# Performance work log

Measured on AMD Instinct MI355X. Metric: run time of the kernel, lower is better.

## Reference

```python
import jax, jax.numpy as jnp
import numpy as np

B, S, LQ = 32, 1024, 128
EMB = 256; H = 256; NH = 8; DH = H // NH
NCATE, NCONT, NNODE = 4, 8, 4
VOCAB = 50000
EPS = 1e-5
LK = S - LQ


def _ln(x, g, b):
    mu = jnp.mean(x, -1, keepdims=True)
    xc = x - mu
    var = jnp.mean(xc * xc, -1, keepdims=True)
    return xc * jax.lax.rsqrt(var + EPS) * g + b


def _leaky(x):
    return jnp.where(x >= 0, x, 0.01 * x)  # LeakyReLU slope 0.01 (torch default)


def setup_inputs() -> dict:
    key = jax.random.key(0)
    ks = jax.random.split(key, 48)
    rnd = lambda i, shape, scale=0.02: jax.random.normal(ks[i], shape, dtype=jnp.float32) * scale
    rng = np.random.default_rng(0)
    qidx = jnp.asarray(np.sort(rng.choice(S, LQ, replace=False)).astype(np.int64))
    cate_table = rnd(6, (VOCAB, EMB)).at[0].set(0.0)  # padding_idx=0
    inp = {
        "node": jax.random.normal(ks[0], (B, S, EMB * NNODE), dtype=jnp.float32),
        "cate": jax.random.randint(ks[1], (B, S, NCATE), 0, VOCAB),
        "cont": jax.random.normal(ks[2], (B, S, NCONT), dtype=jnp.float32),
        "query_index": qidx,
        "mask": jax.random.bernoulli(ks[3], 0.1, (B, LK)),
        "cate_table": cate_table,
        "pos_emb": rnd(4, (1, S, H)),
        "node_W": rnd(5, (EMB * NNODE, H)), "node_b": jnp.zeros((H,), jnp.float32),
        "node_ln_g": jnp.ones((H,), jnp.float32), "node_ln_b": jnp.zeros((H,), jnp.float32),
        "cate_W": rnd(7, (EMB * NCATE, H)), "cate_b": jnp.zeros((H,), jnp.float32),
        "cate_ln_g": jnp.ones((H,), jnp.float32), "cate_ln_b": jnp.zeros((H,), jnp.float32),
        "bn_g": jnp.ones((NCONT,), jnp.float32), "bn_b": jnp.zeros((NCONT,), jnp.float32),
        "cont_W": rnd(8, (NCONT, H)), "cont_b": jnp.zeros((H,), jnp.float32),
        "cont_ln_g": jnp.ones((H,), jnp.float32), "cont_ln_b": jnp.zeros((H,), jnp.float32),
        "comb_W": rnd(9, (3 * H, H)), "comb_b": jnp.zeros((H,), jnp.float32),
        "comb_ln_g": jnp.ones((H,), jnp.float32), "comb_ln_b": jnp.zeros((H,), jnp.float32),
        "q_W": rnd(10, (H, H)), "q_b": jnp.zeros((H,), jnp.float32),
        "k_W": rnd(11, (H, H)), "k_b": jnp.zeros((H,), jnp.float32),
        "v_W": rnd(12, (H, H)), "v_b": jnp.zeros((H,), jnp.float32),
        "reg_W1": rnd(13, (H, H)), "reg_b1": jnp.zeros((H,), jnp.float32),
        "reg_ln_g": jnp.ones((H,), jnp.float32), "reg_ln_b": jnp.zeros((H,), jnp.float32),
        "reg_W2": rnd(14, (H, H)), "reg_b2": jnp.zeros((H,), jnp.float32),
    }
    return inp


def reference(node, cate, cont, query_index, mask, cate_table, pos_emb,
              node_W, node_b, node_ln_g, node_ln_b,
              cate_W, cate_b, cate_ln_g, cate_ln_b,
              bn_g, bn_b, cont_W, cont_b, cont_ln_g, cont_ln_b,
              comb_W, comb_b, comb_ln_g, comb_ln_b,
              q_W, q_b, k_W, k_b, v_W, v_b,
              reg_W1, reg_b1, reg_ln_g, reg_ln_b, reg_W2, reg_b2):
    # --- three embedding branches: Linear -> LayerNorm ---
    node_e = _ln(node @ node_W + node_b, node_ln_g, node_ln_b)
    ce = cate_table[cate].reshape(B, S, NCATE * EMB)  # embedding gather
    cate_e = _ln(ce @ cate_W + cate_b, cate_ln_g, cate_ln_b)
    # BatchNorm1d (training-mode batch stats, biased var) over flattened [B*S, C]
    cf = cont.reshape(-1, NCONT)
    mu = jnp.mean(cf, 0)
    var = jnp.mean((cf - mu) ** 2, 0)
    cn = ((cf - mu) * jax.lax.rsqrt(var + EPS) * bn_g + bn_b).reshape(B, S, NCONT)
    cont_e = _ln(cn @ cont_W + cont_b, cont_ln_g, cont_ln_b)
    # --- combine + positions ---
    seq = jnp.concatenate([node_e, cate_e, cont_e], -1)       # [B,S,3H]
    seq = _ln(_leaky(seq) @ comb_W + comb_b, comb_ln_g, comb_ln_b) + pos_emb  # [B,S,H]
    # --- gather-split cross attention: queries vs complement keys ---
    is_q = jnp.zeros((S,), bool).at[query_index].set(True)
    key_index = jnp.nonzero(~is_q, size=LK)[0]                # setdiff1d, static size
    q = seq[:, query_index]                                   # [B,LQ,H]
    kv = seq[:, key_index]                                    # [B,LK,H]
    Q = (q @ q_W + q_b).reshape(B, LQ, NH, DH).transpose(0, 2, 1, 3)
    K = (kv @ k_W + k_b).reshape(B, LK, NH, DH).transpose(0, 2, 1, 3)
    V = (kv @ v_W + v_b).reshape(B, LK, NH, DH).transpose(0, 2, 1, 3)
    scale = jnp.float32(1.0 / np.sqrt(DH))
    scores = jnp.einsum('bhqd,bhkd->bhqk', Q, K) * scale      # [B,NH,LQ,LK]
    scores = jnp.where(mask[:, None, None, :], jnp.float32(-1e9), scores)
    attn = jax.nn.softmax(scores, -1)                         # dropout = identity (eval)
    out = jnp.einsum('bhqk,bhkd->bhqd', attn, V).transpose(0, 2, 1, 3).reshape(B, LQ, H)
    h = _leaky(_ln(out @ reg_W1 + reg_b1, reg_ln_g, reg_ln_b))
    return h @ reg_W2 + reg_b2                                # [B,LQ,H]
```

## Files before the change

kernel.cpp:

```cpp
#include <hip/hip_runtime.h>
#include <cstdint>

#define EPSV 1e-5f
#define AS1 __attribute__((address_space(1)))
#define AS3 __attribute__((address_space(3)))

#define VMCNT_BAR(N) do { \
    asm volatile("s_waitcnt vmcnt(" #N ") lgkmcnt(0)" ::: "memory"); \
    __builtin_amdgcn_sched_barrier(0); \
    __builtin_amdgcn_s_barrier(); } while (0)

typedef __attribute__((ext_vector_type(8))) short short8v;
typedef __attribute__((ext_vector_type(4))) float float4v;

__device__ inline unsigned short f2bf(float f) {
    union { float f; unsigned int u; } v; v.f = f;
    unsigned int r = v.u + 0x7FFF + ((v.u >> 16) & 1);
    return (unsigned short)(r >> 16);
}

__device__ inline size_t bidx(int n, int k) {
    return ((size_t)(k >> 5) << 13) + ((size_t)(n >> 4) << 9)
         + (((k >> 3) & 3) << 7) + ((n & 15) << 3) + (k & 7);
}

__device__ inline void gld16(const unsigned short* g, unsigned short* d) {
    __builtin_amdgcn_global_load_lds((const AS1 void*)g, (AS3 void*)d, 16, 0, 0);
}

__device__ inline void issue_b(const unsigned short* Bc, int s, unsigned short* bsb,
                               int w, int l) {
    const unsigned short* g = Bc + ((size_t)s << 13) + (w << 9) + (l << 3);
    unsigned short* d = bsb + (w << 9) + (l << 3);
    #pragma unroll
    for (int i = 0; i < 4; ++i)
        gld16(g + (i << 11), d + (i << 11));
}

__device__ inline void issue_b8(const unsigned short* Bc, int s, unsigned short* bsb,
                                int w, int l) {
    const unsigned short* g = Bc + ((size_t)(2 * s) << 13);
    #pragma unroll
    for (int i = 0; i < 4; ++i) {
        int blk = (w + i * 8) << 9;
        gld16(g + blk + (l << 3), bsb + blk + (l << 3));
    }
}

__global__ __launch_bounds__(256) void wt_all_k(
    const float* __restrict__ nW, const float* __restrict__ cW, const float* __restrict__ mW,
    const float* __restrict__ qW, const float* __restrict__ kW, const float* __restrict__ vW,
    const float* __restrict__ r1W, const float* __restrict__ r2W,
    unsigned short* __restrict__ nO, unsigned short* __restrict__ cO, unsigned short* __restrict__ mO,
    unsigned short* __restrict__ qO, unsigned short* __restrict__ kO, unsigned short* __restrict__ vO,
    unsigned short* __restrict__ r1O, unsigned short* __restrict__ r2O)
{
    __shared__ float T[64][65];
    int bid = blockIdx.x;
    const float* W; unsigned short* O; int K, tile;
    if (bid < 64)       { W = nW; O = nO; K = 1024; tile = bid; }
    else if (bid < 128) { W = cW; O = cO; K = 1024; tile = bid - 64; }
    else if (bid < 176) { W = mW; O = mO; K = 768;  tile = bid - 128; }
    else {
        int s = (bid - 176) >> 4; tile = (bid - 176) & 15; K = 256;
        switch (s) {
            case 0: W = qW;  O = qO;  break;
            case 1: W = kW;  O = kO;  break;
            case 2: W = vW;  O = vO;  break;
            case 3: W = r1W; O = r1O; break;
            default: W = r2W; O = r2O; break;
        }
    }
    int kTiles = K >> 6;
    int k0 = (tile % kTiles) * 64, n0 = (tile / kTiles) * 64;
    int c = threadIdx.x & 63, r4 = threadIdx.x >> 6;
    #pragma unroll
    for (int rr = 0; rr < 64; rr += 4) {
        int r = rr + r4;
        T[r][c] = W[(size_t)(k0 + r) * 256 + n0 + c];
    }
    __syncthreads();
    #pragma unroll
    for (int rr = 0; rr < 64; rr += 4) {
        int n = rr + r4;
        O[bidx(n0 + n, k0 + c)] = f2bf(T[c][n]);
    }
}

__global__ __launch_bounds__(512, 4) void gemm_nc_k(
    const float* __restrict__ node, const int* __restrict__ cate,
    const float* __restrict__ table,
    const unsigned short* __restrict__ nWt, const unsigned short* __restrict__ cWt,
    const float* __restrict__ nb, const float* __restrict__ cb,
    const float* __restrict__ nlg, const float* __restrict__ nlb,
    const float* __restrict__ clg, const float* __restrict__ clb,
    unsigned short* __restrict__ Y)
{
    __shared__ union UN {
        unsigned short A[2][4096];
        struct { float S[64][4]; float Q[64][4]; } red;
    } U;
    __shared__ unsigned short Bs[2][16384];
    const int t = threadIdx.x;
    const bool isC = blockIdx.x >= 512;
    const int bm = (isC ? (int)blockIdx.x - 512 : (int)blockIdx.x) * 64;
    const int w = t >> 6, l = t & 63, lr = l & 15, lg = l >> 4;
    const int wm = w >> 2, wn = w & 3;
    const int ar = t >> 3;
    const int ac = (t & 7) * 8;
    const int aw = ((ac >> 5) << 11) + ((ar >> 4) << 9)
                 + (((ac >> 3) & 3) << 7) + ((ar & 15) << 3);

    const unsigned short* Bc = isC ? cWt : nWt;
    const float* bias = isC ? cb : nb;
    const float* lng  = isC ? clg : nlg;
    const float* lnbp = isC ? clb : nlb;
    const int colOff = isC ? 256 : 0;

    const float* apf = node + (size_t)(bm + ar) * 1024 + ac;
    int4 idx4 = {0,0,0,0};
    if (isC) idx4 = *(const int4*)&cate[(bm + ar) * 4];

    float4v acc[2][4];
    #pragma unroll
    for (int i = 0; i < 2; ++i)
        #pragma unroll
        for (int j = 0; j < 4; ++j) acc[i][j] = (float4v)0.f;

    float4 rA0, rA1;

    auto loadA = [&](int s) {
        const float* p;
        if (isC) {
            int kt = s * 64 + ac;
            int g = kt >> 8;
            int idx = (g == 0) ? idx4.x : (g == 1) ? idx4.y : (g == 2) ? idx4.z : idx4.w;
            p = table + (size_t)idx * 256 + (kt & 255);
        } else {
            p = apf + s * 64;
        }
        rA0 = *(const float4*)p;
        rA1 = *(const float4*)(p + 4);
    };
    auto writeA = [&](unsigned short* Ab) {
        short8v v;
        v[0] = (short)f2bf(rA0.x); v[1] = (short)f2bf(rA0.y);
        v[2] = (short)f2bf(rA0.z); v[3] = (short)f2bf(rA0.w);
        v[4] = (short)f2bf(rA1.x); v[5] = (short)f2bf(rA1.y);
        v[6] = (short)f2bf(rA1.z); v[7] = (short)f2bf(rA1.w);
        *(short8v*)&Ab[aw] = v;
    };
    auto comp = [&](const unsigned short* Ab, const unsigned short* bsb) {
        #pragma unroll
        for (int kk = 0; kk < 2; ++kk) {
            short8v af[2], bf[4];
            #pragma unroll
            for (int i = 0; i < 2; ++i)
                af[i] = *(const short8v*)&Ab[kk*2048 + ((wm*2 + i) << 9) + (lg << 7) + (lr << 3)];
            #pragma unroll
            for (int j = 0; j < 4; ++j)
                bf[j] = *(const short8v*)&bsb[kk*8192 + ((wn*4 + j) << 9) + (lg << 7) + (lr << 3)];
            #pragma unroll
            for (int i = 0; i < 2; ++i)
                #pragma unroll
                for (int j = 0; j < 4; ++j)
                    acc[i][j] = __builtin_amdgcn_mfma_f32_16x16x32_bf16(af[i], bf[j], acc[i][j], 0, 0, 0);
        }
    };

    issue_b8(Bc, 0, &Bs[0][0], w, l);
    loadA(0);
    writeA(U.A[0]);
    VMCNT_BAR(0);

    for (int s = 0; s < 16; ++s) {
        const int cur = s & 1;
        if (s + 1 < 16) {
            issue_b8(Bc, s + 1, &Bs[1 - cur][0], w, l);
            loadA(s + 1);
        }
        __builtin_amdgcn_sched_barrier(0);
        comp(U.A[cur], &Bs[cur][0]);
        if (s + 1 < 16) {
            writeA(U.A[1 - cur]);
            VMCNT_BAR(0);
        }
    }

    #pragma unroll
    for (int j = 0; j < 4; ++j) {
        float bvj = bias[wn*64 + j*16 + lr];
        #pragma unroll
        for (int i = 0; i < 2; ++i)
            #pragma unroll
            for (int r4 = 0; r4 < 4; ++r4) acc[i][j][r4] += bvj;
    }
    __syncthreads();
    #pragma unroll
    for (int i = 0; i < 2; ++i) {
        float ps[4], qs[4];
        #pragma unroll
        for (int r4 = 0; r4 < 4; ++r4) {
            float a0 = acc[i][0][r4], a1 = acc[i][1][r4],
                  a2 = acc[i][2][r4], a3 = acc[i][3][r4];
            ps[r4] = (a0 + a1) + (a2 + a3);
            qs[r4] = (a0*a0 + a1*a1) + (a2*a2 + a3*a3);
        }
        #pragma unroll
        for (int o = 1; o < 16; o <<= 1)
            #pragma unroll
            for (int r4 = 0; r4 < 4; ++r4) {
                ps[r4] += __shfl_xor(ps[r4], o);
                qs[r4] += __shfl_xor(qs[r4], o);
            }
        if (lr == 0) {
            #pragma unroll
            for (int r4 = 0; r4 < 4; ++r4) {
                int rlc = wm*32 + i*16 + lg*4 + r4;
                U.red.S[rlc][wn] = ps[r4];
                U.red.Q[rlc][wn] = qs[r4];
            }
        }
    }
    __syncthreads();
    #pragma unroll
    for (int i = 0; i < 2; ++i) {
        float mu[4], rstd[4];
        #pragma unroll
        for (int r4 = 0; r4 < 4; ++r4) {
            int rlc = wm*32 + i*16 + lg*4 + r4;
            float s  = (U.red.S[rlc][0] + U.red.S[rlc][1]) + (U.red.S[rlc][2] + U.red.S[rlc][3]);
            float qq = (U.red.Q[rlc][0] + U.red.Q[rlc][1]) + (U.red.Q[rlc][2] + U.red.Q[rlc][3]);
            float m_ = s * (1.0f/256.0f);
            mu[r4] = m_;
            rstd[r4] = rsqrtf(qq * (1.0f/256.0f) - m_*m_ + EPSV);
        }
        #pragma unroll
        for (int j = 0; j < 4; ++j) {
            int c = wn*64 + j*16 + lr;
            float gv = lng[c], b2 = lnbp[c];
            #pragma unroll
            for (int r4 = 0; r4 < 4; ++r4) {
                int row = bm + wm*32 + i*16 + lg*4 + r4;
                float y = (acc[i][j][r4] - mu[r4]) * rstd[r4] * gv + b2;
                y = (y >= 0.f) ? y : 0.01f*y;
                Y[(size_t)row * 768 + colOff + c] = f2bf(y);
            }
        }
    }
}

__global__ __launch_bounds__(512, 4) void gemm_comb_k(
    const unsigned short* __restrict__ A,
    const unsigned short* __restrict__ Bc,
    const float* __restrict__ bias,
    const float* __restrict__ lng, const float* __restrict__ lnbp,
    const float* __restrict__ pos,
    unsigned short* __restrict__ Y)
{
    __shared__ union UC {
        unsigned short A[2][4096];
        struct { float S[64][4]; float Q[64][4]; } red;
    } U;
    __shared__ unsigned short Bs[2][16384];
    const int t = threadIdx.x;
    const int bm = blockIdx.x * 64;
    const int w = t >> 6, l = t & 63, lr = l & 15, lg = l >> 4;
    const int wm = w >> 2, wn = w & 3;
    const int ar = t >> 3;
    const int ak = (t & 7) * 8;
    const int aw = ((ak >> 5) << 11) + ((ar >> 4) << 9)
                 + (((ak >> 3) & 3) << 7) + ((ar & 15) << 3);

    const unsigned short* ap = A + (size_t)(bm + ar) * 768 + ak;

    float4v acc[2][4];
    #pragma unroll
    for (int i = 0; i < 2; ++i)
        #pragma unroll
        for (int j = 0; j < 4; ++j) acc[i][j] = (float4v)0.f;

    short8v aA;

    auto comp = [&](const unsigned short* Ab, const unsigned short* bsb) {
        #pragma unroll
        for (int kk = 0; kk < 2; ++kk) {
            short8v af[2], bf[4];
            #pragma unroll
            for (int i = 0; i < 2; ++i)
                af[i] = *(const short8v*)&Ab[kk*2048 + ((wm*2 + i) << 9) + (lg << 7) + (lr << 3)];
            #pragma unroll
            for (int j = 0; j < 4; ++j)
                bf[j] = *(const short8v*)&bsb[kk*8192 + ((wn*4 + j) << 9) + (lg << 7) + (lr << 3)];
            #pragma unroll
            for (int i = 0; i < 2; ++i)
                #pragma unroll
                for (int j = 0; j < 4; ++j)
                    acc[i][j] = __builtin_amdgcn_mfma_f32_16x16x32_bf16(af[i], bf[j], acc[i][j], 0, 0, 0);
        }
    };

    issue_b8(Bc, 0, &Bs[0][0], w, l);
    aA = *(const short8v*)(ap);
    *(short8v*)&U.A[0][aw] = aA;
    VMCNT_BAR(0);

    for (int s = 0; s < 12; ++s) {
        const int cur = s & 1;
        if (s + 1 < 12) {
            issue_b8(Bc, s + 1, &Bs[1 - cur][0], w, l);
            aA = *(const short8v*)(ap + (s + 1) * 64);
        }
        __builtin_amdgcn_sched_barrier(0);
        comp(U.A[cur], &Bs[cur][0]);
        if (s + 1 < 12) {
            *(short8v*)&U.A[1 - cur][aw] = aA;
            VMCNT_BAR(0);
        }
    }

    #pragma unroll
    for (int j = 0; j < 4; ++j) {
        float bvj = bias[wn*64 + j*16 + lr];
        #pragma unroll
        for (int i = 0; i < 2; ++i)
            #pragma unroll
            for (int r4 = 0; r4 < 4; ++r4) acc[i][j][r4] += bvj;
    }
    __syncthreads();
    #pragma unroll
    for (int i = 0; i < 2; ++i) {
        float ps[4], qs[4];
        #pragma unroll
        for (int r4 = 0; r4 < 4; ++r4) {
            float a0 = acc[i][0][r4], a1 = acc[i][1][r4],
                  a2 = acc[i][2][r4], a3 = acc[i][3][r4];
            ps[r4] = (a0 + a1) + (a2 + a3);
            qs[r4] = (a0*a0 + a1*a1) + (a2*a2 + a3*a3);
        }
        #pragma unroll
        for (int o = 1; o < 16; o <<= 1)
            #pragma unroll
            for (int r4 = 0; r4 < 4; ++r4) {
                ps[r4] += __shfl_xor(ps[r4], o);
                qs[r4] += __shfl_xor(qs[r4], o);
            }
        if (lr == 0) {
            #pragma unroll
            for (int r4 = 0; r4 < 4; ++r4) {
                int rlc = wm*32 + i*16 + lg*4 + r4;
                U.red.S[rlc][wn] = ps[r4];
                U.red.Q[rlc][wn] = qs[r4];
            }
        }
    }
    __syncthreads();
    #pragma unroll
    for (int i = 0; i < 2; ++i) {
        float mu[4], rstd[4];
        #pragma unroll
        for (int r4 = 0; r4 < 4; ++r4) {
            int rlc = wm*32 + i*16 + lg*4 + r4;
            float s  = (U.red.S[rlc][0] + U.red.S[rlc][1]) + (U.red.S[rlc][2] + U.red.S[rlc][3]);
            float qq = (U.red.Q[rlc][0] + U.red.Q[rlc][1]) + (U.red.Q[rlc][2] + U.red.Q[rlc][3]);
            float m_ = s * (1.0f/256.0f);
            mu[r4] = m_;
            rstd[r4] = rsqrtf(qq * (1.0f/256.0f) - m_*m_ + EPSV);
        }
        #pragma unroll
        for (int j = 0; j < 4; ++j) {
            int c = wn*64 + j*16 + lr;
            float gv = lng[c], b2 = lnbp[c];
            #pragma unroll
            for (int r4 = 0; r4 < 4; ++r4) {
                int row = bm + wm*32 + i*16 + lg*4 + r4;
                float y = (acc[i][j][r4] - mu[r4]) * rstd[r4] * gv + b2
                        + pos[(size_t)(row & 1023) * 256 + c];
                Y[(size_t)row * 256 + c] = f2bf(y);
            }
        }
    }
}

__global__ __launch_bounds__(512, 4) void gemm_qkv_k(
    const unsigned short* __restrict__ seq,
    const int* __restrict__ qmap, const int* __restrict__ krmap,
    const unsigned short* __restrict__ qWt, const unsigned short* __restrict__ kWt,
    const unsigned short* __restrict__ vWt,
    const float* __restrict__ qb, const float* __restrict__ kb, const float* __restrict__ vb,
    unsigned short* __restrict__ Qo, unsigned short* __restrict__ Ko,
    unsigned short* __restrict__ Vt)
{
    __shared__ unsigned short Asl[2][4096];
    __shared__ unsigned short Bs[2][16384];
    const int t = threadIdx.x;
    const int bid = blockIdx.x;
    int seg, bm;
    const int* gmap; const unsigned short* Bc; const float* bias;
    if (bid < 64)       { seg = 0; bm = bid * 64;         gmap = qmap;  Bc = qWt; bias = qb; }
    else if (bid < 512) { seg = 1; bm = (bid - 64) * 64;  gmap = krmap; Bc = kWt; bias = kb; }
    else                { seg = 2; bm = (bid - 512) * 64; gmap = krmap; Bc = vWt; bias = vb; }
    const int w = t >> 6, l = t & 63, lr = l & 15, lg = l >> 4;
    const int wm = w >> 2, wn = w & 3;
    const int ar = t >> 3;
    const int ak = (t & 7) * 8;
    const int aw = ((ak >> 5) << 11) + ((ar >> 4) << 9)
                 + (((ak >> 3) & 3) << 7) + ((ar & 15) << 3);

    const unsigned short* ap = seq + (size_t)gmap[bm + ar] * 256 + ak;

    float4v acc[2][4];
    #pragma unroll
    for (int i = 0; i < 2; ++i)
        #pragma unroll
        for (int j = 0; j < 4; ++j) acc[i][j] = (float4v)0.f;

    short8v aA;

    auto comp = [&](const unsigned short* Ab, const unsigned short* bsb) {
        #pragma unroll
        for (int kk = 0; kk < 2; ++kk) {
            short8v af[2], bf[4];
            #pragma unroll
            for (int i = 0; i < 2; ++i)
                af[i] = *(const short8v*)&Ab[kk*2048 + ((wm*2 + i) << 9) + (lg << 7) + (lr << 3)];
            #pragma unroll
            for (int j = 0; j < 4; ++j)
                bf[j] = *(const short8v*)&bsb[kk*8192 + ((wn*4 + j) << 9) + (lg << 7) + (lr << 3)];
            #pragma unroll
            for (int i = 0; i < 2; ++i)
                #pragma unroll
                for (int j = 0; j < 4; ++j)
                    acc[i][j] = __builtin_amdgcn_mfma_f32_16x16x32_bf16(af[i], bf[j], acc[i][j], 0, 0, 0);
        }
    };

    issue_b8(Bc, 0, &Bs[0][0], w, l);
    aA = *(const short8v*)(ap);
    *(short8v*)&Asl[0][aw] = aA;
    VMCNT_BAR(0);

    for (int s = 0; s < 4; ++s) {
        const int cur = s & 1;
        if (s + 1 < 4) {
            issue_b8(Bc, s + 1, &Bs[1 - cur][0], w, l);
            aA = *(const short8v*)(ap + (s + 1) * 64);
        }
        __builtin_amdgcn_sched_barrier(0);
        comp(Asl[cur], &Bs[cur][0]);
        if (s + 1 < 4) {
            *(short8v*)&Asl[1 - cur][aw] = aA;
            VMCNT_BAR(0);
        }
    }

    unsigned short* outp = (seg == 0) ? Qo : (seg == 1) ? Ko : Vt;
    #pragma unroll
    for (int j = 0; j < 4; ++j) {
        int c = wn*64 + j*16 + lr;
        float bvj = bias[c];
        #pragma unroll
        for (int i = 0; i < 2; ++i) {
            #pragma unroll
            for (int r4 = 0; r4 < 4; ++r4) {
                int rl = wm*32 + i*16 + lg*4 + r4;
                float val = acc[i][j][r4] + bvj;
                if (seg < 2) {
                    outp[(size_t)(bm + rl) * 256 + c] = f2bf(val);
                } else {
                    int vbk = bm / 896;
                    int kl = bm - vbk * 896 + rl;
                    outp[((size_t)vbk * 256 + c) * 896 + kl] = f2bf(val);
                }
            }
        }
    }
}

template<int EPI>
__global__ __launch_bounds__(256) void gemm_reg_k(
    const unsigned short* __restrict__ Asrc,
    const unsigned short* __restrict__ Bc,
    const float* __restrict__ bias,
    const float* __restrict__ ln_g,
    const float* __restrict__ ln_b,
    void* __restrict__ Cout)
{
    __shared__ union UR {
        unsigned short A[2][4096];
        struct { float S[64][4]; float Q[64][4]; } red;
    } U;
    __shared__ unsigned short Bs[2][16384];
    const int t = threadIdx.x;
    const int bm = blockIdx.x * 64;
    const int w = t >> 6, l = t & 63, lr = l & 15, lg = l >> 4;
    const int ar = t >> 2;
    const int ac = (t & 3) * 16;
    const int aw0 = (((t & 3) >> 1) << 11) + ((ar >> 4) << 9)
                  + ((((t & 3) * 2) & 3) << 7) + ((ar & 15) << 3);
    const int aw1 = aw0 + 128;

    const unsigned short* ap = Asrc + (size_t)(bm + ar) * 256 + ac;

    float4v acc[4][4];
    #pragma unroll
    for (int i = 0; i < 4; ++i)
        #pragma unroll
        for (int j = 0; j < 4; ++j) acc[i][j] = (float4v)0.f;

    short8v a0A, a1A, a0B, a1B;

    auto comp = [&](const unsigned short* Ab, const unsigned short* bsb) {
        #pragma unroll
        for (int kk = 0; kk < 2; ++kk) {
            short8v af[4], bf[4];
            #pragma unroll
            for (int i = 0; i < 4; ++i)
                af[i] = *(const short8v*)&Ab[kk*2048 + i*512 + lg*128 + lr*8];
            #pragma unroll
            for (int j = 0; j < 4; ++j)
                bf[j] = *(const short8v*)&bsb[kk*8192 + ((w*4 + j) << 9) + (lg << 7) + (lr << 3)];
            #pragma unroll
            for (int i = 0; i < 4; ++i)
                #pragma unroll
                for (int j = 0; j < 4; ++j)
                    acc[i][j] = __builtin_amdgcn_mfma_f32_16x16x32_bf16(af[i], bf[j], acc[i][j], 0, 0, 0);
        }
    };

    issue_b(Bc, 0, &Bs[0][0], w, l);
    issue_b(Bc, 1, &Bs[0][8192], w, l);
    a0A = *(const short8v*)(ap);
    a1A = *(const short8v*)(ap + 8);
    for (int s = 0; s < 4; ++s) {
        int cur = s & 1;
        __syncthreads();
        *(short8v*)&U.A[cur][aw0] = a0A;
        *(short8v*)&U.A[cur][aw1] = a1A;
        __syncthreads();
        if (s + 1 < 4) {
            issue_b(Bc, 2*(s+1),     &Bs[1 - cur][0],    w, l);
            issue_b(Bc, 2*(s+1) + 1, &Bs[1 - cur][8192], w, l);
            a0B = *(const short8v*)(ap + (s + 1) * 64);
            a1B = *(const short8v*)(ap + (s + 1) * 64 + 8);
        }
        comp(U.A[cur], &Bs[cur][0]);
        a0A = a0B; a1A = a1B;
    }

    #pragma unroll
    for (int j = 0; j < 4; ++j) {
        float bvj = bias[w*64 + j*16 + lr];
        #pragma unroll
        for (int i = 0; i < 4; ++i)
            #pragma unroll
            for (int r4 = 0; r4 < 4; ++r4) acc[i][j][r4] += bvj;
    }

    if (EPI == 0) {
        #pragma unroll
        for (int i = 0; i < 4; ++i)
            #pragma unroll
            for (int j = 0; j < 4; ++j) {
                int c = w*64 + j*16 + lr;
                #pragma unroll
                for (int r4 = 0; r4 < 4; ++r4) {
                    int rl = i*16 + lg*4 + r4;
                    ((float*)Cout)[(size_t)(bm + rl) * 256 + c] = acc[i][j][r4];
                }
            }
    } else {
        __syncthreads();
        #pragma unroll
        for (int i = 0; i < 4; ++i) {
            float ps[4], qs[4];
            #pragma unroll
            for (int r4 = 0; r4 < 4; ++r4) {
                float a0 = acc[i][0][r4], a1 = acc[i][1][r4],
                      a2 = acc[i][2][r4], a3 = acc[i][3][r4];
                ps[r4] = (a0 + a1) + (a2 + a3);
                qs[r4] = (a0*a0 + a1*a1) + (a2*a2 + a3*a3);
            }
            #pragma unroll
            for (int o = 1; o < 16; o <<= 1)
                #pragma unroll
                for (int r4 = 0; r4 < 4; ++r4) {
                    ps[r4] += __shfl_xor(ps[r4], o);
                    qs[r4] += __shfl_xor(qs[r4], o);
                }
            if (lr == 0) {
                #pragma unroll
                for (int r4 = 0; r4 < 4; ++r4) {
                    U.red.S[i*16 + lg*4 + r4][w] = ps[r4];
                    U.red.Q[i*16 + lg*4 + r4][w] = qs[r4];
                }
            }
        }
        __syncthreads();
        #pragma unroll
        for (int i = 0; i < 4; ++i) {
            float mu[4], rstd[4];
            #pragma unroll
            for (int r4 = 0; r4 < 4; ++r4) {
                int rl = i*16 + lg*4 + r4;
                float s  = (U.red.S[rl][0] + U.red.S[rl][1]) + (U.red.S[rl][2] + U.red.S[rl][3]);
                float qq = (U.red.Q[rl][0] + U.red.Q[rl][1]) + (U.red.Q[rl][2] + U.red.Q[rl][3]);
                float m_ = s * (1.0f/256.0f);
                mu[r4] = m_;
                rstd[r4] = rsqrtf(qq * (1.0f/256.0f) - m_*m_ + EPSV);
            }
            #pragma unroll
            for (int j = 0; j < 4; ++j) {
                int c = w*64 + j*16 + lr;
                float gv = ln_g[c], b2 = ln_b[c];
                #pragma unroll
                for (int r4 = 0; r4 < 4; ++r4) {
                    int row = bm + i*16 + lg*4 + r4;
                    float y = (acc[i][j][r4] - mu[r4]) * rstd[r4] * gv + b2;
                    y = (y >= 0.f) ? y : 0.01f*y;
                    ((unsigned short*)Cout)[(size_t)row * 256 + c] = f2bf(y);
                }
            }
        }
    }
}

__global__ __launch_bounds__(256) void bn_stats_k(const float* __restrict__ cont,
                                                  float* __restrict__ stats)
{
    __shared__ float ss[8], sq[8];
    int tid = threadIdx.x;
    if (tid < 8) { ss[tid] = 0.f; sq[tid] = 0.f; }
    __syncthreads();
    int gt = blockIdx.x * 256 + tid;
    float s = 0.f, q = 0.f;
    for (int e = gt; e < 32768*8; e += 256*256) { float v = cont[e]; s += v; q += v*v; }
    int f = gt & 7;
    atomicAdd(&ss[f], s);
    atomicAdd(&sq[f], q);
    __syncthreads();
    if (tid < 8) { atomicAdd(&stats[tid], ss[tid]); atomicAdd(&stats[8+tid], sq[tid]); }
}

__global__ __launch_bounds__(256) void cont_k(
    const float* __restrict__ cont, const float* __restrict__ stats,
    const float* __restrict__ bn_g, const float* __restrict__ bn_b,
    const float* __restrict__ W, const float* __restrict__ bias,
    const float* __restrict__ g, const float* __restrict__ bL,
    unsigned short* __restrict__ seq3)
{
    __shared__ float Ws[8][256];
    __shared__ float sscale[8], sshift[8];
    __shared__ float cr[8];
    __shared__ float red[8];
    int tid = threadIdx.x;
    #pragma unroll
    for (int d = 0; d < 8; ++d) Ws[d][tid] = W[d*256 + tid];
    if (tid < 8) {
        float mean = stats[tid] * (1.0f/32768.0f);
        float var  = stats[8+tid] * (1.0f/32768.0f) - mean*mean;
        float r = rsqrtf(var + EPSV);
        float sc = r * bn_g[tid];
        sscale[tid] = sc;
        sshift[tid] = bn_b[tid] - mean*sc;
    }
    __syncthreads();
    int lane = tid & 63, wv = tid >> 6;
    float gv = g[tid], bv = bL[tid], biasv = bias[tid];
    for (int row = blockIdx.x; row < 32768; row += gridDim.x) {
        if (tid < 8) cr[tid] = cont[(size_t)row*8 + tid]*sscale[tid] + sshift[tid];
        __syncthreads();
        float acc = biasv;
        #pragma unroll
        for (int d = 0; d < 8; ++d) acc += cr[d]*Ws[d][tid];
        float s = acc;
        #pragma unroll
        for (int o = 32; o; o >>= 1) s += __shfl_xor(s, o);
        if (lane == 0) red[wv] = s;
        __syncthreads();
        float mu = (red[0]+red[1]+red[2]+red[3]) * (1.0f/256.0f);
        float dc = acc - mu;
        float qv = dc*dc;
        #pragma unroll
        for (int o = 32; o; o >>= 1) qv += __shfl_xor(qv, o);
        if (lane == 0) red[4+wv] = qv;
        __syncthreads();
        float var = (red[4]+red[5]+red[6]+red[7]) * (1.0f/256.0f);
        float y = dc * rsqrtf(var + EPSV) * gv + bv;
        y = (y >= 0.f) ? y : 0.01f*y;
        seq3[(size_t)row*768 + 512 + tid] = f2bf(y);
        __syncthreads();
    }
}

__global__ void build_maps_k(const int* __restrict__ qidx, int* __restrict__ kmap)
{
    __shared__ int flag[1024];
    __shared__ int scan[1024];
    int t = threadIdx.x;
    flag[t] = 0;
    __syncthreads();
    if (t < 128) flag[qidx[t]] = 1;
    __syncthreads();
    int nq = 1 - flag[t];
    scan[t] = nq;
    __syncthreads();
    for (int off = 1; off < 1024; off <<= 1) {
        int v = (t >= off) ? scan[t - off] : 0;
        __syncthreads();
        scan[t] += v;
        __syncthreads();
    }
    if (nq) kmap[scan[t] - 1] = t;
}

__global__ void expand_maps_k(const int* __restrict__ qidx, const int* __restrict__ kmap,
                              int* __restrict__ qmap, int* __restrict__ krmap)
{
    int i = blockIdx.x * 256 + threadIdx.x;
    if (i < 32*128) { int b = i >> 7; int t = i & 127; qmap[i] = b*1024 + qidx[t]; }
    if (i < 32*896) { int b = i / 896; int t = i - b*896; krmap[i] = b*1024 + kmap[t]; }
}

__global__ __launch_bounds__(256) void mask_sniff_k(const unsigned char* __restrict__ msrc,
                                                    int* __restrict__ flags)
{
    int i = blockIdx.x * 256 + threadIdx.x;
    unsigned char v = msrc[i];
    bool u8  = v && (i & 3);
    bool i32 = v && !(i & 3) && ((i & 7) == 4);
    unsigned long long bu = __ballot(u8);
    unsigned long long bi = __ballot(i32);
    if ((threadIdx.x & 63) == 0) {
        if (bu) atomicOr(&flags[0], 1);
        if (bi) atomicOr(&flags[1], 1);
    }
}

__global__ __launch_bounds__(256) void mask_conv_k(const unsigned char* __restrict__ msrc,
                                                   const int* __restrict__ flags,
                                                   unsigned char* __restrict__ mu8)
{
    int i = blockIdx.x * 256 + threadIdx.x;
    int mode = flags[0] ? 0 : (flags[1] ? 1 : 2);
    unsigned char v;
    if (mode == 0)      v = msrc[i] ? 1 : 0;
    else if (mode == 1) v = ((const int*)msrc)[i] ? 1 : 0;
    else                v = ((const long long*)msrc)[i] ? 1 : 0;
    mu8[i] = v;
}

__global__ __launch_bounds__(256) void attn_mfma_k(
    const unsigned short* __restrict__ Qb,
    const unsigned short* __restrict__ Kb,
    const unsigned short* __restrict__ Vtb,
    const unsigned char* __restrict__ mask,
    unsigned short* __restrict__ out)
{
    __shared__ unsigned short Pw[4][16][72];
    const int t = threadIdx.x;
    const int w = t >> 6, l = t & 63;
    const int lr = l & 15, lg = l >> 4;
    const int bx = blockIdx.x;
    const int qh = bx & 1, h = (bx >> 1) & 7, b = bx >> 4;
    const int qrow0 = b*128 + qh*64 + w*16;

    short8v qf = *(const short8v*)&Qb[(size_t)(qrow0 + lr)*256 + h*32 + lg*8];

    const unsigned short* Kbase = Kb + (size_t)b*896*256 + h*32;
    const unsigned short* Vbase = Vtb + ((size_t)b*256 + h*32)*896;
    const unsigned char* mrow = mask + b*896;

    float4v O0 = (float4v)0.f, O1 = (float4v)0.f;
    float m[4], lsum[4];
    #pragma unroll
    for (int r = 0; r < 4; ++r) { m[r] = -3.0e38f; lsum[r] = 0.f; }

    short8v kf[4], vf[4];
    int mk[4];
    #pragma unroll
    for (int i = 0; i < 4; ++i) {
        kf[i] = *(const short8v*)&Kbase[(size_t)(i*16 + lr)*256 + lg*8];
        mk[i] = mrow[i*16 + lr];
    }
    #pragma unroll
    for (int kc = 0; kc < 2; ++kc)
        #pragma unroll
        for (int nt = 0; nt < 2; ++nt)
            vf[kc*2+nt] = *(const short8v*)&Vbase[(size_t)(nt*16 + lr)*896 + kc*32 + lg*8];

    for (int kt3 = 0; kt3 < 14; ++kt3) {
        const int kb2 = kt3*64 + 64;
        short8v kf2[4], vf2[4];
        int mk2[4];
        if (kt3 < 13) {
            #pragma unroll
            for (int i = 0; i < 4; ++i) {
                kf2[i] = *(const short8v*)&Kbase[(size_t)(kb2 + i*16 + lr)*256 + lg*8];
                mk2[i] = mrow[kb2 + i*16 + lr];
            }
            #pragma unroll
            for (int kc = 0; kc < 2; ++kc)
                #pragma unroll
                for (int nt = 0; nt < 2; ++nt)
                    vf2[kc*2+nt] = *(const short8v*)&Vbase[(size_t)(nt*16 + lr)*896 + kb2 + kc*32 + lg*8];
        }
        float4v s4[4];
        #pragma unroll
        for (int i = 0; i < 4; ++i)
            s4[i] = __builtin_amdgcn_mfma_f32_16x16x32_bf16(qf, kf[i], (float4v)0.f, 0, 0, 0);
        #pragma unroll
        for (int i = 0; i < 4; ++i)
            #pragma unroll
            for (int r = 0; r < 4; ++r)
                s4[i][r] = mk[i] ? -1e9f : s4[i][r] * 0.17677669529663687f;
        float tm[4];
        #pragma unroll
        for (int r = 0; r < 4; ++r)
            tm[r] = fmaxf(fmaxf(s4[0][r], s4[1][r]), fmaxf(s4[2][r], s4[3][r]));
        #pragma unroll
        for (int o = 1; o < 16; o <<= 1)
            #pragma unroll
            for (int r = 0; r < 4; ++r) tm[r] = fmaxf(tm[r], __shfl_xor(tm[r], o));
        float resc[4];
        #pragma unroll
        for (int r = 0; r < 4; ++r) {
            float mn = fmaxf(m[r], tm[r]);
            resc[r] = __expf(m[r] - mn);
            m[r] = mn;
        }
        float rs[4] = {0.f, 0.f, 0.f, 0.f};
        #pragma unroll
        for (int i = 0; i < 4; ++i)
            #pragma unroll
            for (int r = 0; r < 4; ++r) {
                float p = __expf(s4[i][r] - m[r]);
                s4[i][r] = p;
                rs[r] += p;
            }
        #pragma unroll
        for (int o = 1; o < 16; o <<= 1)
            #pragma unroll
            for (int r = 0; r < 4; ++r) rs[r] += __shfl_xor(rs[r], o);
        #pragma unroll
        for (int r = 0; r < 4; ++r) lsum[r] = lsum[r]*resc[r] + rs[r];
        #pragma unroll
        for (int r = 0; r < 4; ++r) { O0[r] *= resc[r]; O1[r] *= resc[r]; }
        #pragma unroll
        for (int i = 0; i < 4; ++i)
            #pragma unroll
            for (int r = 0; r < 4; ++r)
                Pw[w][lg*4 + r][i*16 + lr] = f2bf(s4[i][r]);
        #pragma unroll
        for (int kc = 0; kc < 2; ++kc) {
            short8v pf = *(const short8v*)&Pw[w][lr][kc*32 + lg*8];
            O0 = __builtin_amdgcn_mfma_f32_16x16x32_bf16(pf, vf[kc*2+0], O0, 0, 0, 0);
            O1 = __builtin_amdgcn_mfma_f32_16x16x32_bf16(pf, vf[kc*2+1], O1, 0, 0, 0);
        }
        if (kt3 < 13) {
            #pragma unroll
            for (int i = 0; i < 4; ++i) { kf[i] = kf2[i]; mk[i] = mk2[i]; vf[i] = vf2[i]; }
        }
    }
    #pragma unroll
    for (int r = 0; r < 4; ++r) {
        float inv = 1.0f / lsum[r];
        size_t row = (size_t)(qrow0 + lg*4 + r);
        out[row*256 + h*32 + lr]      = f2bf(O0[r] * inv);
        out[row*256 + h*32 + 16 + lr] = f2bf(O1[r] * inv);
    }
}

extern "C" void kernel_launch(void* const* d_in, const int* in_sizes, int n_in,
                              void* d_out, int out_size, void* d_ws, size_t ws_size,
                              hipStream_t stream)
{
    const float* node       = (const float*)d_in[0];
    const int*   cate       = (const int*)d_in[1];
    const float* cont       = (const float*)d_in[2];
    const int*   qidx       = (const int*)d_in[3];
    const unsigned char* mask = (const unsigned char*)d_in[4];
    const float* cate_table = (const float*)d_in[5];
    const float* pos_emb    = (const float*)d_in[6];
    const float* node_W     = (const float*)d_in[7];
    const float* node_b     = (const float*)d_in[8];
    const float* node_ln_g  = (const float*)d_in[9];
    const float* node_ln_b  = (const float*)d_in[10];
    const float* cate_W     = (const float*)d_in[11];
    const float* cate_b     = (const float*)d_in[12];
    const float* cate_ln_g  = (const float*)d_in[13];
    const float* cate_ln_b  = (const float*)d_in[14];
    const float* bn_g       = (const float*)d_in[15];
    const float* bn_b       = (const float*)d_in[16];
    const float* cont_W     = (const float*)d_in[17];
    const float* cont_b     = (const float*)d_in[18];
    const float* cont_ln_g  = (const float*)d_in[19];
    const float* cont_ln_b  = (const float*)d_in[20];
    const float* comb_W     = (const float*)d_in[21];
    const float* comb_b     = (const float*)d_in[22];
    const float* comb_ln_g  = (const float*)d_in[23];
    const float* comb_ln_b  = (const float*)d_in[24];
    const float* q_W        = (const float*)d_in[25];
    const float* q_b        = (const float*)d_in[26];
    const float* k_W        = (const float*)d_in[27];
    const float* k_b        = (const float*)d_in[28];
    const float* v_W        = (const float*)d_in[29];
    const float* v_b        = (const float*)d_in[30];
    const float* reg_W1     = (const float*)d_in[31];
    const float* reg_b1     = (const float*)d_in[32];
    const float* reg_ln_g   = (const float*)d_in[33];
    const float* reg_ln_b   = (const float*)d_in[34];
    const float* reg_W2     = (const float*)d_in[35];
    const float* reg_b2     = (const float*)d_in[36];

    char* ws = (char*)d_ws;
    unsigned short* seq3bf = (unsigned short*)(ws + 0);
    unsigned short* seqbf  = (unsigned short*)(ws + 83886080);
    unsigned short* Qbf    = (unsigned short*)(ws + 100663296);
    unsigned short* Kbf    = (unsigned short*)(ws + 102760448);
    unsigned short* Vtbf   = (unsigned short*)(ws + 117440512);
    unsigned short* AObf   = (unsigned short*)(ws + 132120576);
    unsigned short* Hbf    = (unsigned short*)(ws + 0);
    float* stats = (float*)(ws + 165675008);
    int*   flags = (int*)  (ws + 165675072);
    int*   kmap  = (int*)  (ws + 165675136);
    int*   qmap  = (int*)  (ws + 165678720);
    int*   krmap = (int*)  (ws + 165695104);
    unsigned char* mu8 = (unsigned char*)(ws + 165809792);
    unsigned short* node_Wt = (unsigned short*)(ws + 165838464);
    unsigned short* cate_Wt = (unsigned short*)(ws + 166362752);
    unsigned short* comb_Wt = (unsigned short*)(ws + 166887040);
    unsigned short* q_Wt    = (unsigned short*)(ws + 167280256);
    unsigned short* k_Wt    = (unsigned short*)(ws + 167411328);
    unsigned short* v_Wt    = (unsigned short*)(ws + 167542400);
    unsigned short* r1_Wt   = (unsigned short*)(ws + 167673472);
    unsigned short* r2_Wt   = (unsigned short*)(ws + 167804544);
    float* outp = (float*)d_out;

    hipMemsetAsync(stats, 0, 128, stream);
    bn_stats_k<<<256, 256, 0, stream>>>(cont, stats);
    mask_sniff_k<<<112, 256, 0, stream>>>(mask, flags);
    mask_conv_k<<<112, 256, 0, stream>>>(mask, flags, mu8);
    wt_all_k<<<256, 256, 0, stream>>>(node_W, cate_W, comb_W, q_W, k_W, v_W, reg_W1, reg_W2,
                                      node_Wt, cate_Wt, comb_Wt, q_Wt, k_Wt, v_Wt, r1_Wt, r2_Wt);

    gemm_nc_k<<<1024, 512, 0, stream>>>(node, cate, cate_table, node_Wt, cate_Wt,
        node_b, cate_b, node_ln_g, node_ln_b, cate_ln_g, cate_ln_b, seq3bf);
    cont_k<<<2048, 256, 0, stream>>>(cont, stats, bn_g, bn_b, cont_W, cont_b,
                                     cont_ln_g, cont_ln_b, seq3bf);
    gemm_comb_k<<<512, 512, 0, stream>>>(seq3bf, comb_Wt, comb_b,
        comb_ln_g, comb_ln_b, pos_emb, seqbf);
    build_maps_k<<<1, 1024, 0, stream>>>(qidx, kmap);
    expand_maps_k<<<112, 256, 0, stream>>>(qidx, kmap, qmap, krmap);
    gemm_qkv_k<<<960, 512, 0, stream>>>(seqbf, qmap, krmap, q_Wt, k_Wt, v_Wt,
        q_b, k_b, v_b, Qbf, Kbf, Vtbf);
    attn_mfma_k<<<512, 256, 0, stream>>>(Qbf, Kbf, Vtbf, mu8, AObf);
    gemm_reg_k<3><<<64, 256, 0, stream>>>(AObf, r1_Wt, reg_b1, reg_ln_g, reg_ln_b, Hbf);
    gemm_reg_k<0><<<64, 256, 0, stream>>>(Hbf, r2_Wt, reg_b2, nullptr, nullptr, outp);
}
```

Measured before the change: 250.5 us.

## Triple-buffer node/cate GEMM with direct-to-LDS fp32 A loads and K=32 stages

The node/cate projection GEMM now loads fp32 A tiles straight into LDS with global_load_lds instead of staging them in registers. The bf16 conversion moves to fragment-read time inside the compute step. The K loop changes from 16 double-buffered stages of 64 to 32 triple-buffered stages of 32, keeping two stages of loads in flight behind a partial vmcnt wait. This targets the exposed load latency and register staging of the old loop, at the cost of more barriers, repeated per-wave bf16 conversions, and different LDS usage.

```diff
diff --git a/kernel.cpp b/kernel.cpp
--- a/kernel.cpp
+++ b/kernel.cpp
@@ -27,6 +27,9 @@
 __device__ inline void gld16(const unsigned short* g, unsigned short* d) {
     __builtin_amdgcn_global_load_lds((const AS1 void*)g, (AS3 void*)d, 16, 0, 0);
 }
+__device__ inline void gld16f(const float* g, float* d) {
+    __builtin_amdgcn_global_load_lds((const AS1 void*)g, (AS3 void*)d, 16, 0, 0);
+}
 
 __device__ inline void issue_b(const unsigned short* Bc, int s, unsigned short* bsb,
                                int w, int l) {
@@ -42,6 +45,16 @@
     const unsigned short* g = Bc + ((size_t)(2 * s) << 13);
     #pragma unroll
     for (int i = 0; i < 4; ++i) {
+        int blk = (w + i * 8) << 9;
+        gld16(g + blk + (l << 3), bsb + blk + (l << 3));
+    }
+}
+
+__device__ inline void issue_b32(const unsigned short* Bc, int s, unsigned short* bsb,
+                                 int w, int l) {
+    const unsigned short* g = Bc + ((size_t)s << 13);
+    #pragma unroll
+    for (int i = 0; i < 2; ++i) {
         int blk = (w + i * 8) << 9;
         gld16(g + blk + (l << 3), bsb + blk + (l << 3));
     }
@@ -97,19 +110,17 @@
     unsigned short* __restrict__ Y)
 {
     __shared__ union UN {
-        unsigned short A[2][4096];
+        float Af[3][2048];
         struct { float S[64][4]; float Q[64][4]; } red;
     } U;
-    __shared__ unsigned short Bs[2][16384];
+    __shared__ unsigned short Bs[3][8192];
     const int t = threadIdx.x;
     const bool isC = blockIdx.x >= 512;
     const int bm = (isC ? (int)blockIdx.x - 512 : (int)blockIdx.x) * 64;
     const int w = t >> 6, l = t & 63, lr = l & 15, lg = l >> 4;
     const int wm = w >> 2, wn = w & 3;
-    const int ar = t >> 3;
-    const int ac = (t & 7) * 8;
-    const int aw = ((ac >> 5) << 11) + ((ar >> 4) << 9)
-                 + (((ac >> 3) & 3) << 7) + ((ar & 15) << 3);
+    const int grow = ((t >> 7) << 4) | ((t >> 1) & 15);
+    const int gk   = (((t >> 5) & 3) << 3) | ((t & 1) << 2);
 
     const unsigned short* Bc = isC ? cWt : nWt;
     const float* bias = isC ? cb : nb;
@@ -117,9 +128,9 @@
     const float* lnbp = isC ? clb : nlb;
     const int colOff = isC ? 256 : 0;
 
-    const float* apf = node + (size_t)(bm + ar) * 1024 + ac;
+    const float* apf = node + (size_t)(bm + grow) * 1024 + gk;
     int4 idx4 = {0,0,0,0};
-    if (isC) idx4 = *(const int4*)&cate[(bm + ar) * 4];
+    if (isC) idx4 = *(const int4*)&cate[(bm + grow) * 4];
 
     float4v acc[2][4];
     #pragma unroll
@@ -127,63 +138,57 @@
         #pragma unroll
         for (int j = 0; j < 4; ++j) acc[i][j] = (float4v)0.f;
 
-    float4 rA0, rA1;
-
-    auto loadA = [&](int s) {
+    auto issue_a = [&](int s, int buf) {
         const float* p;
         if (isC) {
-            int kt = s * 64 + ac;
-            int g = kt >> 8;
+            int g = s >> 3;
             int idx = (g == 0) ? idx4.x : (g == 1) ? idx4.y : (g == 2) ? idx4.z : idx4.w;
-            p = table + (size_t)idx * 256 + (kt & 255);
+            p = table + (size_t)idx * 256 + ((s & 7) * 32 + gk);
         } else {
-            p = apf + s * 64;
-        }
-        rA0 = *(const float4*)p;
-        rA1 = *(const float4*)(p + 4);
+            p = apf + s * 32;
+        }
+        gld16f(p, &U.Af[buf][t << 2]);
     };
-    auto writeA = [&](unsigned short* Ab) {
-        short8v v;
-        v[0] = (short)f2bf(rA0.x); v[1] = (short)f2bf(rA0.y);
-        v[2] = (short)f2bf(rA0.z); v[3] = (short)f2bf(rA0.w);
-        v[4] = (short)f2bf(rA1.x); v[5] = (short)f2bf(rA1.y);
-        v[6] = (short)f2bf(rA1.z); v[7] = (short)f2bf(rA1.w);
-        *(short8v*)&Ab[aw] = v;
+    auto comp = [&](const float* Afb, const unsigned short* bsb) {
+        short8v af[2], bf[4];
+        #pragma unroll
+        for (int i = 0; i < 2; ++i) {
+            const float* fp = &Afb[((wm*2 + i) << 9) + (lg << 7) + (lr << 3)];
+            float4 x0 = *(const float4*)fp;
+            float4 x1 = *(const float4*)(fp + 4);
+            af[i][0] = (short)f2bf(x0.x); af[i][1] = (short)f2bf(x0.y);
+            af[i][2] = (short)f2bf(x0.z); af[i][3] = (short)f2bf(x0.w);
+            af[i][4] = (short)f2bf(x1.x); af[i][5] = (short)f2bf(x1.y);
+            af[i][6] = (short)f2bf(x1.z); af[i][7] = (short)f2bf(x1.w);
+        }
+        #pragma unroll
+        for (int j = 0; j < 4; ++j)
+            bf[j] = *(const short8v*)&bsb[((wn*4 + j) << 9) + (lg << 7) + (lr << 3)];
+        #pragma unroll
+        for (int i = 0; i < 2; ++i)
+            #pragma unroll
+            for (int j = 0; j < 4; ++j)
+                acc[i][j] = __builtin_amdgcn_mfma_f32_16x16x32_bf16(af[i], bf[j], acc[i][j], 0, 0, 0);
     };
-    auto comp = [&](const unsigned short* Ab, const unsigned short* bsb) {
-        #pragma unroll
-        for (int kk = 0; kk < 2; ++kk) {
-            short8v af[2], bf[4];
-            #pragma unroll
-            for (int i = 0; i < 2; ++i)
-                af[i] = *(const short8v*)&Ab[kk*2048 + ((wm*2 + i) << 9) + (lg << 7) + (lr << 3)];
-            #pragma unroll
-            for (int j = 0; j < 4; ++j)
-                bf[j] = *(const short8v*)&bsb[kk*8192 + ((wn*4 + j) << 9) + (lg << 7) + (lr << 3)];
-            #pragma unroll
-            for (int i = 0; i < 2; ++i)
-                #pragma unroll
-                for (int j = 0; j < 4; ++j)
-                    acc[i][j] = __builtin_amdgcn_mfma_f32_16x16x32_bf16(af[i], bf[j], acc[i][j], 0, 0, 0);
-        }
-    };
-
-    issue_b8(Bc, 0, &Bs[0][0], w, l);
-    loadA(0);
-    writeA(U.A[0]);
-    VMCNT_BAR(0);
-
-    for (int s = 0; s < 16; ++s) {
-        const int cur = s & 1;
-        if (s + 1 < 16) {
-            issue_b8(Bc, s + 1, &Bs[1 - cur][0], w, l);
-            loadA(s + 1);
+
+    issue_b32(Bc, 0, &Bs[0][0], w, l);
+    issue_a(0, 0);
+    issue_b32(Bc, 1, &Bs[1][0], w, l);
+    issue_a(1, 1);
+    VMCNT_BAR(3);
+
+    for (int s = 0; s < 32; ++s) {
+        const int cur = s % 3;
+        if (s + 2 < 32) {
+            const int nb3 = (s + 2) % 3;
+            issue_b32(Bc, s + 2, &Bs[nb3][0], w, l);
+            issue_a(s + 2, nb3);
         }
         __builtin_amdgcn_sched_barrier(0);
-        comp(U.A[cur], &Bs[cur][0]);
-        if (s + 1 < 16) {
-            writeA(U.A[1 - cur]);
-            VMCNT_BAR(0);
+        comp(U.Af[cur], &Bs[cur][0]);
+        if (s + 1 < 32) {
+            if (s + 2 < 32) VMCNT_BAR(3);
+            else            VMCNT_BAR(0);
         }
     }
 
```

Result: slower. 265.3 us (+5.9%).
